# Optimization experiments

Hardware: AMD Instinct MI355X
Metric: run time of the kernel (lower is better)

## Reference

```python
import jax, jax.numpy as jnp
import numpy as np

N_NODES = 50000
N_EDGES = 800000
HIDDEN = 128
HEADS = 8
HEAD_DIM = HIDDEN // HEADS
N_REL = 64
SCALE = np.sqrt(HEAD_DIM).astype(np.float32)


def setup_inputs() -> dict:
    key = jax.random.key(0)
    ks = jax.random.split(key, 12)
    s = 1.0 / np.sqrt(2 * HIDDEN)
    s2 = 1.0 / np.sqrt(HIDDEN)
    return {
        "node_features": jax.random.normal(ks[0], (N_NODES, HIDDEN), jnp.float32),
        "query_embedding": jax.random.normal(ks[1], (1, HIDDEN), jnp.float32),
        "relation_embeddings": jax.random.normal(ks[2], (N_REL, HIDDEN), jnp.float32),
        "Wq": jax.random.uniform(ks[3], (2 * HIDDEN, HIDDEN), jnp.float32, -s, s),
        "bq": jnp.zeros((HIDDEN,), jnp.float32),
        "Wk": jax.random.uniform(ks[4], (2 * HIDDEN, HIDDEN), jnp.float32, -s, s),
        "bk": jnp.zeros((HIDDEN,), jnp.float32),
        "Wv": jax.random.uniform(ks[5], (HIDDEN, HIDDEN), jnp.float32, -s2, s2),
        "bv": jnp.zeros((HIDDEN,), jnp.float32),
        "Wo": jax.random.uniform(ks[6], (HIDDEN, HIDDEN), jnp.float32, -s2, s2),
        "bo": jnp.zeros((HIDDEN,), jnp.float32),
        "edge_index": jax.random.randint(ks[7], (2, N_EDGES), 0, N_NODES, jnp.int64),
        "edge_type": jax.random.randint(ks[8], (N_EDGES,), 0, N_REL, jnp.int64),
    }


def reference(node_features, query_embedding, relation_embeddings,
              Wq, bq, Wk, bk, Wv, bv, Wo, bo, edge_index, edge_type):
    n = node_features.shape[0]
    # expand query to all nodes and concat: [N, 2*hidden]
    q_exp = jnp.broadcast_to(query_embedding, (n, HIDDEN))
    nq = jnp.concatenate([node_features, q_exp], axis=-1)
    q = (nq @ Wq + bq).reshape(n, HEADS, HEAD_DIM)
    k = (nq @ Wk + bk).reshape(n, HEADS, HEAD_DIM)
    v = (node_features @ Wv + bv).reshape(n, HEADS, HEAD_DIM)

    src, dst = edge_index[0], edge_index[1]
    rel_bias = relation_embeddings[edge_type].reshape(-1, HEADS, HEAD_DIM)

    # edge-wise scores [E, heads]
    scores = jnp.sum(q[dst] * (k[src] + rel_bias), axis=-1) / SCALE

    # sparse softmax grouped by dst; torch init of max buffer is 0 -> clamp at 0
    seg_max = jax.ops.segment_max(scores, dst, num_segments=n)
    seg_max = jnp.maximum(seg_max, 0.0)
    exp_s = jnp.exp(scores - seg_max[dst])
    seg_sum = jax.ops.segment_sum(exp_s, dst, num_segments=n)
    attn = exp_s / (seg_sum[dst] + 1e-8)  # [E, heads]

    messages = attn[:, :, None] * v[src]  # [E, heads, head_dim]
    out = jax.ops.segment_sum(messages, dst, num_segments=n)  # [N, heads, head_dim]
    out = out.reshape(n, HIDDEN)
    return out @ Wo + bo
```

## Files before the change

### kernel.cpp

```cpp
#include <hip/hip_runtime.h>
#include <math.h>

#define N_NODES 50000
#define N_EDGES 800000
#define HID 128
#define HEADS 8
#define HDIM 16
#define CAP 96
#define CNT_BLOCKS 3125
#define QKV_BLOCKS 782
#define NFB_BLOCKS 3125

typedef __attribute__((ext_vector_type(8))) short short8;
typedef __attribute__((ext_vector_type(4))) float floatx4;

#if defined(__has_builtin)
#if __has_builtin(__builtin_amdgcn_fdot2_f32_bf16)
#define HAVE_DOT2 1
#endif
#endif
#ifndef HAVE_DOT2
#define HAVE_DOT2 0
#endif

#if HAVE_DOT2
typedef __attribute__((ext_vector_type(2))) __bf16 bf16x2;
__device__ __forceinline__ float dot2acc(unsigned int a, unsigned int b, float c) {
    return __builtin_amdgcn_fdot2_f32_bf16(__builtin_bit_cast(bf16x2, a),
                                           __builtin_bit_cast(bf16x2, b), c, false);
}
#endif

__device__ __forceinline__ float bf_lo(unsigned int d) { return __uint_as_float(d << 16); }
__device__ __forceinline__ float bf_hi(unsigned int d) { return __uint_as_float(d & 0xFFFF0000u); }
__device__ __forceinline__ unsigned short f2bf(float f) {
    unsigned int u = __float_as_uint(f);
    u = (u + 0x7FFFu + ((u >> 16) & 1u)) >> 16;
    return (unsigned short)u;
}
__device__ __forceinline__ unsigned int pack_bf2(float a, float b) {
    return (unsigned int)f2bf(a) | ((unsigned int)f2bf(b) << 16);
}

__global__ __launch_bounds__(256) void prep_kernel(
    const float* __restrict__ nf,
    const float* __restrict__ query, const float* __restrict__ rel,
    const float* __restrict__ Wq, const float* __restrict__ bq,
    const float* __restrict__ Wk, const float* __restrict__ bk,
    const float* __restrict__ Wv, const float* __restrict__ Wo,
    unsigned short* __restrict__ Wt, unsigned short* __restrict__ relbf,
    int* __restrict__ counts, float* __restrict__ bqe, float* __restrict__ bke,
    unsigned short* __restrict__ nfb) {
    __shared__ float fred[256];
    int b = blockIdx.x, tid = threadIdx.x;
    if (b >= 258) {
        int base = (b - 258) * 2048 + tid * 8;
        const float4* p = (const float4*)(nf + base);
        float4 a0 = p[0], a1 = p[1];
        short8 f;
        f[0] = (short)f2bf(a0.x); f[1] = (short)f2bf(a0.y);
        f[2] = (short)f2bf(a0.z); f[3] = (short)f2bf(a0.w);
        f[4] = (short)f2bf(a1.x); f[5] = (short)f2bf(a1.y);
        f[6] = (short)f2bf(a1.z); f[7] = (short)f2bf(a1.w);
        *(short8*)(nfb + base) = f;
        return;
    }
    if (b >= 256) {
        const float* W  = (b == 256) ? Wq : Wk;
        const float* bb = (b == 256) ? bq : bk;
        float* dst      = (b == 256) ? bqe : bke;
        int j = tid & 127;
        int half = tid >> 7;
        float a = 0.0f;
        int i0 = half * 64;
        for (int i = 0; i < 64; ++i) a += query[i0 + i] * W[(HID + i0 + i) * HID + j];
        fred[tid] = a;
        __syncthreads();
        if (half == 0) dst[j] = fred[j] + fred[128 + j] + bb[j];
        return;
    }
    int idx = b * 256 + tid;
    if (idx < N_NODES) counts[idx] = 0;
    if (idx < 64 * HID) relbf[idx] = f2bf(rel[idx]);
    int m = idx >> 14;
    int rem = idx & 16383;
    int n = rem >> 7, k = rem & 127;
    const float* W = (m == 0) ? Wq : (m == 1) ? Wk : (m == 2) ? Wv : Wo;
    Wt[idx] = f2bf(W[k * HID + n]);
}

__global__ __launch_bounds__(256) void bucket_kernel(
    const int* __restrict__ ei, const int* __restrict__ et,
    int* __restrict__ counts, unsigned int* __restrict__ slots) {
    int e = blockIdx.x * 256 + threadIdx.x;
    if (e < N_EDGES) {
        int dst = ei[N_EDGES + e];
        int pos = atomicAdd(&counts[dst], 1);
        if (pos < CAP)
            slots[(unsigned)dst * CAP + pos] =
                ((unsigned int)et[e] << 18) | (unsigned int)ei[e];
    }
}

__global__ __launch_bounds__(256) void qkv_kernel(
    const unsigned short* __restrict__ nfb, const unsigned short* __restrict__ Wt,
    const float* __restrict__ bqe, const float* __restrict__ bke, const float* __restrict__ bv,
    unsigned short* __restrict__ qb16, unsigned short* __restrict__ kv16) {
    int row0 = blockIdx.x * 64;
    int wave = threadIdx.x >> 6;
    int lane = threadIdx.x & 63;
    int col  = lane & 15;
    int quad = lane >> 4;

    short8 afr[4][4];
    #pragma unroll
    for (int t = 0; t < 4; ++t) {
        int arow = row0 + t * 16 + col;
        int asafe = (arow < N_NODES) ? arow : (N_NODES - 1);
        #pragma unroll
        for (int kk = 0; kk < 4; ++kk)
            afr[t][kk] = *(const short8*)(nfb + (size_t)asafe * HID + kk * 32 + quad * 8);
    }
    const float* biases[3] = {bqe, bke, bv};
    #pragma unroll
    for (int m = 0; m < 3; ++m) {
        const unsigned short* W = Wt + (size_t)m * HID * HID;
        #pragma unroll
        for (int nn = 0; nn < 2; ++nn) {
            int n = wave * 2 + nn;
            float b = biases[m][n * 16 + col];
            floatx4 acc[4];
            #pragma unroll
            for (int t = 0; t < 4; ++t) acc[t] = (floatx4){b, b, b, b};
            short8 bfr[4];
            #pragma unroll
            for (int kk = 0; kk < 4; ++kk)
                bfr[kk] = *(const short8*)(W + (size_t)(n * 16 + col) * HID + kk * 32 + quad * 8);
            #pragma unroll
            for (int kk = 0; kk < 4; ++kk)
                #pragma unroll
                for (int t = 0; t < 4; ++t)
                    acc[t] = __builtin_amdgcn_mfma_f32_16x16x32_bf16(afr[t][kk], bfr[kk], acc[t], 0, 0, 0);
            #pragma unroll
            for (int t = 0; t < 4; ++t) {
                #pragma unroll
                for (int i = 0; i < 4; ++i) {
                    int r = row0 + t * 16 + quad * 4 + i;
                    if (r < N_NODES) {
                        int c = n * 16 + col;
                        if (m == 0)      qb16[(size_t)r * HID + c] = f2bf(acc[t][i]);
                        else if (m == 1) kv16[(size_t)r * 256 + c] = f2bf(acc[t][i]);
                        else             kv16[(size_t)r * 256 + 128 + c] = f2bf(acc[t][i]);
                    }
                }
            }
        }
    }
}

__global__ __launch_bounds__(256) void attn_kernel(
    const unsigned int* __restrict__ qb, const unsigned int* __restrict__ kvu,
    const unsigned int* __restrict__ relu,
    const int* __restrict__ counts, const unsigned int* __restrict__ slots,
    unsigned int* __restrict__ abuf) {
    int node = blockIdx.x * 4 + (threadIdx.x >> 6);
    int lane = threadIdx.x & 63;
    int h = lane & 7;
    int hd = lane >> 3;
    int deg = counts[node];
    if (deg > CAP) deg = CAP;
    unsigned int rs = (unsigned)node * CAP;

    const uint4* qp = (const uint4*)(qb + (unsigned)node * 64 + h * 8);
    uint4 qa = qp[0], qc = qp[1];
#if !HAVE_DOT2
    float qf0 = bf_lo(qa.x), qf1 = bf_hi(qa.x), qf2 = bf_lo(qa.y), qf3 = bf_hi(qa.y);
    float qf4 = bf_lo(qa.z), qf5 = bf_hi(qa.z), qf6 = bf_lo(qa.w), qf7 = bf_hi(qa.w);
    float qf8 = bf_lo(qc.x), qf9 = bf_hi(qc.x), qf10 = bf_lo(qc.y), qf11 = bf_hi(qc.y);
    float qf12 = bf_lo(qc.z), qf13 = bf_hi(qc.z), qf14 = bf_lo(qc.w), qf15 = bf_hi(qc.w);
#endif

    int myel = hd;
    unsigned int pk = (myel < deg) ? slots[rs + myel] : 0u;
    float ssum = 0.0f, accx = 0.0f, accy = 0.0f;
    for (int base = 0; base < deg; base += 8) {
        int el = base + myel;
        int eln = el + 8;
        unsigned int pk_next = (eln < deg) ? slots[rs + eln] : 0u;
        unsigned int pw = 0u;
        if (el < deg) {
            unsigned int src = pk & 0x3FFFF;
            unsigned int etv = pk >> 18;
            const uint4* kp = (const uint4*)(kvu + (src << 7) + h * 8);
            uint4 ka = kp[0], kb = kp[1];
            const uint4* rp = (const uint4*)(relu + (etv << 6) + h * 8);
            uint4 ra = rp[0], rb = rp[1];
            float s;
#if HAVE_DOT2
            float s0 = dot2acc(qa.x, ka.x, 0.0f);
            float s1 = dot2acc(qa.y, ka.y, 0.0f);
            float s2 = dot2acc(qa.z, ka.z, 0.0f);
            float s3 = dot2acc(qa.w, ka.w, 0.0f);
            s0 = dot2acc(qc.x, kb.x, s0);
            s1 = dot2acc(qc.y, kb.y, s1);
            s2 = dot2acc(qc.z, kb.z, s2);
            s3 = dot2acc(qc.w, kb.w, s3);
            s0 = dot2acc(qa.x, ra.x, s0);
            s1 = dot2acc(qa.y, ra.y, s1);
            s2 = dot2acc(qa.z, ra.z, s2);
            s3 = dot2acc(qa.w, ra.w, s3);
            s0 = dot2acc(qc.x, rb.x, s0);
            s1 = dot2acc(qc.y, rb.y, s1);
            s2 = dot2acc(qc.z, rb.z, s2);
            s3 = dot2acc(qc.w, rb.w, s3);
            s = (s0 + s1) + (s2 + s3);
#else
            float s0 = qf0 * (bf_lo(ka.x) + bf_lo(ra.x)) + qf4 * (bf_lo(ka.z) + bf_lo(ra.z))
                     + qf8 * (bf_lo(kb.x) + bf_lo(rb.x)) + qf12 * (bf_lo(kb.z) + bf_lo(rb.z));
            float s1 = qf1 * (bf_hi(ka.x) + bf_hi(ra.x)) + qf5 * (bf_hi(ka.z) + bf_hi(ra.z))
                     + qf9 * (bf_hi(kb.x) + bf_hi(rb.x)) + qf13 * (bf_hi(kb.z) + bf_hi(rb.z));
            float s2 = qf2 * (bf_lo(ka.y) + bf_lo(ra.y)) + qf6 * (bf_lo(ka.w) + bf_lo(ra.w))
                     + qf10 * (bf_lo(kb.y) + bf_lo(rb.y)) + qf14 * (bf_lo(kb.w) + bf_lo(rb.w));
            float s3 = qf3 * (bf_hi(ka.y) + bf_hi(ra.y)) + qf7 * (bf_hi(ka.w) + bf_hi(ra.w))
                     + qf11 * (bf_hi(kb.y) + bf_hi(rb.y)) + qf15 * (bf_hi(kb.w) + bf_hi(rb.w));
            s = (s0 + s1) + (s2 + s3);
#endif
            float w = __expf(s * 0.25f);
            unsigned int wb = (unsigned int)f2bf(w);
            ssum += __uint_as_float(wb << 16);
            pw = (wb << 16) | src;
        }
        #pragma unroll
        for (int j = 0; j < 8; ++j) {
            unsigned int pj = __shfl(pw, j * 8 + hd);
            float wj = bf_hi(pj);
            unsigned int sj = pj & 0xFFFFu;
            unsigned int vp = kvu[(sj << 7) + 64 + lane];
            accx += wj * bf_lo(vp);
            accy += wj * bf_hi(vp);
        }
        pk = pk_next;
    }
    #pragma unroll
    for (int off = 8; off < 64; off <<= 1) ssum += __shfl_xor(ssum, off);
    float inv = 1.0f / (__shfl(ssum, hd) + 1e-8f);
    abuf[(unsigned)node * 64 + lane] = pack_bf2(accx * inv, accy * inv);
}

__global__ __launch_bounds__(256) void out_mfma_kernel(
    const unsigned short* __restrict__ abuf, const unsigned short* __restrict__ Wot,
    const float* __restrict__ bo, float* __restrict__ out) {
    int row0 = blockIdx.x * 64;
    int wave = threadIdx.x >> 6;
    int lane = threadIdx.x & 63;
    int col  = lane & 15;
    int quad = lane >> 4;

    short8 afr[4][4];
    #pragma unroll
    for (int t = 0; t < 4; ++t) {
        int arow = row0 + t * 16 + col;
        int asafe = (arow < N_NODES) ? arow : (N_NODES - 1);
        #pragma unroll
        for (int kk = 0; kk < 4; ++kk)
            afr[t][kk] = *(const short8*)(abuf + (size_t)asafe * HID + kk * 32 + quad * 8);
    }

    #pragma unroll
    for (int nn = 0; nn < 2; ++nn) {
        int n = wave * 2 + nn;
        float b = bo[n * 16 + col];
        floatx4 acc[4];
        #pragma unroll
        for (int t = 0; t < 4; ++t) acc[t] = (floatx4){b, b, b, b};
        short8 bfr[4];
        #pragma unroll
        for (int kk = 0; kk < 4; ++kk)
            bfr[kk] = *(const short8*)(Wot + (size_t)(n * 16 + col) * HID + kk * 32 + quad * 8);
        #pragma unroll
        for (int kk = 0; kk < 4; ++kk)
            #pragma unroll
            for (int t = 0; t < 4; ++t)
                acc[t] = __builtin_amdgcn_mfma_f32_16x16x32_bf16(afr[t][kk], bfr[kk], acc[t], 0, 0, 0);
        #pragma unroll
        for (int t = 0; t < 4; ++t) {
            #pragma unroll
            for (int i = 0; i < 4; ++i) {
                int r = row0 + t * 16 + quad * 4 + i;
                if (r < N_NODES) out[(size_t)r * HID + n * 16 + col] = acc[t][i];
            }
        }
    }
}

extern "C" void kernel_launch(void* const* d_in, const int* in_sizes, int n_in,
                              void* d_out, int out_size, void* d_ws, size_t ws_size,
                              hipStream_t stream) {
    const float* nf    = (const float*)d_in[0];
    const float* query = (const float*)d_in[1];
    const float* rel   = (const float*)d_in[2];
    const float* Wq    = (const float*)d_in[3];
    const float* bq    = (const float*)d_in[4];
    const float* Wk    = (const float*)d_in[5];
    const float* bk    = (const float*)d_in[6];
    const float* Wv    = (const float*)d_in[7];
    const float* bv    = (const float*)d_in[8];
    const float* Wo    = (const float*)d_in[9];
    const float* bo    = (const float*)d_in[10];
    const int*   ei    = (const int*)d_in[11];
    const int*   et    = (const int*)d_in[12];
    float* out = (float*)d_out;

    char* ws = (char*)d_ws;
    unsigned short* qb16 = (unsigned short*)ws; ws += (size_t)N_NODES * HID * 2;
    unsigned short* kv16 = (unsigned short*)ws; ws += (size_t)N_NODES * 256 * 2;
    unsigned int* abuf   = (unsigned int*)ws;   ws += (size_t)N_NODES * 64 * 4;
    float* bqe           = (float*)ws;          ws += 128 * 4;
    float* bke           = (float*)ws;          ws += 128 * 4;
    int* counts          = (int*)ws;            ws += (size_t)N_NODES * 4;
    unsigned int* slots  = (unsigned int*)ws;   ws += (size_t)N_NODES * CAP * 4;
    unsigned short* Wt   = (unsigned short*)ws; ws += (size_t)4 * HID * HID * 2;
    unsigned short* relbf = (unsigned short*)ws; ws += (size_t)64 * HID * 2;
    unsigned short* nfb  = (unsigned short*)ws; ws += (size_t)N_NODES * HID * 2;

    prep_kernel<<<258 + NFB_BLOCKS, 256, 0, stream>>>(nf, query, rel, Wq, bq, Wk, bk, Wv, Wo,
                                                      Wt, relbf, counts, bqe, bke, nfb);
    bucket_kernel<<<CNT_BLOCKS, 256, 0, stream>>>(ei, et, counts, slots);
    qkv_kernel<<<QKV_BLOCKS, 256, 0, stream>>>(nfb, Wt, bqe, bke, bv, qb16, kv16);
    attn_kernel<<<N_NODES / 4, 256, 0, stream>>>(
        (const unsigned int*)qb16, (const unsigned int*)kv16,
        (const unsigned int*)relbf, counts, slots, abuf);
    out_mfma_kernel<<<QKV_BLOCKS, 256, 0, stream>>>(
        (const unsigned short*)abuf, Wt + (size_t)3 * HID * HID, bo, out);
}
```

Measured before the change: 251.0 us.

## Fuse edge bucketing into prep kernel and vectorize attention V gather

Merges the edge bucketing pass into the prep kernel, with each thread handling four edges through int4 loads, and clears the counts buffer with a memset instead of inside prep. In the attention kernel, each lane now gathers 16 bytes of V per edge instead of 4, and partial sums are reduced across lane quarters with shuffles, with a single uint4 store per row. The goal is to cut one kernel launch, use wider memory transactions and shorten the per-edge gather loop. The cost is extra shuffle reductions and more accumulator registers, and bucket atomics now run concurrently with the conversion blocks.

Measured after the change: 246.5 us. No clear change (-1.8%).

```diff
diff --git a/kernel.cpp b/kernel.cpp
--- a/kernel.cpp
+++ b/kernel.cpp
@@ -7,9 +7,9 @@
 #define HEADS 8
 #define HDIM 16
 #define CAP 96
-#define CNT_BLOCKS 3125
 #define QKV_BLOCKS 782
 #define NFB_BLOCKS 3125
+#define BUCKET_BLOCKS 782
 
 typedef __attribute__((ext_vector_type(8))) short short8;
 typedef __attribute__((ext_vector_type(4))) float floatx4;
@@ -42,19 +42,40 @@
     return (unsigned int)f2bf(a) | ((unsigned int)f2bf(b) << 16);
 }
 
-__global__ __launch_bounds__(256) void prep_kernel(
+__global__ __launch_bounds__(256) void prep_bucket_kernel(
     const float* __restrict__ nf,
     const float* __restrict__ query, const float* __restrict__ rel,
     const float* __restrict__ Wq, const float* __restrict__ bq,
     const float* __restrict__ Wk, const float* __restrict__ bk,
     const float* __restrict__ Wv, const float* __restrict__ Wo,
+    const int* __restrict__ ei, const int* __restrict__ et,
+    int* __restrict__ counts, unsigned int* __restrict__ slots,
     unsigned short* __restrict__ Wt, unsigned short* __restrict__ relbf,
-    int* __restrict__ counts, float* __restrict__ bqe, float* __restrict__ bke,
+    float* __restrict__ bqe, float* __restrict__ bke,
     unsigned short* __restrict__ nfb) {
     __shared__ float fred[256];
     int b = blockIdx.x, tid = threadIdx.x;
-    if (b >= 258) {
-        int base = (b - 258) * 2048 + tid * 8;
+    if (b < BUCKET_BLOCKS) {
+        int t4 = b * 256 + tid;
+        if (t4 < N_EDGES / 4) {
+            int e0 = t4 * 4;
+            int4 dd = *(const int4*)(ei + N_EDGES + e0);
+            int4 ss = *(const int4*)(ei + e0);
+            int4 tt = *(const int4*)(et + e0);
+            int p0 = atomicAdd(&counts[dd.x], 1);
+            int p1 = atomicAdd(&counts[dd.y], 1);
+            int p2 = atomicAdd(&counts[dd.z], 1);
+            int p3 = atomicAdd(&counts[dd.w], 1);
+            if (p0 < CAP) slots[(unsigned)dd.x * CAP + p0] = ((unsigned)tt.x << 18) | (unsigned)ss.x;
+            if (p1 < CAP) slots[(unsigned)dd.y * CAP + p1] = ((unsigned)tt.y << 18) | (unsigned)ss.y;
+            if (p2 < CAP) slots[(unsigned)dd.z * CAP + p2] = ((unsigned)tt.z << 18) | (unsigned)ss.z;
+            if (p3 < CAP) slots[(unsigned)dd.w * CAP + p3] = ((unsigned)tt.w << 18) | (unsigned)ss.w;
+        }
+        return;
+    }
+    b -= BUCKET_BLOCKS;
+    if (b < NFB_BLOCKS) {
+        int base = b * 2048 + tid * 8;
         const float4* p = (const float4*)(nf + base);
         float4 a0 = p[0], a1 = p[1];
         short8 f;
@@ -65,7 +86,18 @@
         *(short8*)(nfb + base) = f;
         return;
     }
-    if (b >= 256) {
+    b -= NFB_BLOCKS;
+    if (b < 256) {
+        int idx = b * 256 + tid;
+        if (idx < 64 * HID) relbf[idx] = f2bf(rel[idx]);
+        int m = idx >> 14;
+        int rem = idx & 16383;
+        int n = rem >> 7, k = rem & 127;
+        const float* W = (m == 0) ? Wq : (m == 1) ? Wk : (m == 2) ? Wv : Wo;
+        Wt[idx] = f2bf(W[k * HID + n]);
+        return;
+    }
+    {
         const float* W  = (b == 256) ? Wq : Wk;
         const float* bb = (b == 256) ? bq : bk;
         float* dst      = (b == 256) ? bqe : bke;
@@ -77,28 +109,6 @@
         fred[tid] = a;
         __syncthreads();
         if (half == 0) dst[j] = fred[j] + fred[128 + j] + bb[j];
-        return;
-    }
-    int idx = b * 256 + tid;
-    if (idx < N_NODES) counts[idx] = 0;
-    if (idx < 64 * HID) relbf[idx] = f2bf(rel[idx]);
-    int m = idx >> 14;
-    int rem = idx & 16383;
-    int n = rem >> 7, k = rem & 127;
-    const float* W = (m == 0) ? Wq : (m == 1) ? Wk : (m == 2) ? Wv : Wo;
-    Wt[idx] = f2bf(W[k * HID + n]);
-}
-
-__global__ __launch_bounds__(256) void bucket_kernel(
-    const int* __restrict__ ei, const int* __restrict__ et,
-    int* __restrict__ counts, unsigned int* __restrict__ slots) {
-    int e = blockIdx.x * 256 + threadIdx.x;
-    if (e < N_EDGES) {
-        int dst = ei[N_EDGES + e];
-        int pos = atomicAdd(&counts[dst], 1);
-        if (pos < CAP)
-            slots[(unsigned)dst * CAP + pos] =
-                ((unsigned int)et[e] << 18) | (unsigned int)ei[e];
     }
 }
 
@@ -167,6 +177,8 @@
     int lane = threadIdx.x & 63;
     int h = lane & 7;
     int hd = lane >> 3;
+    int qi = lane & 15;
+    int quarter = lane >> 4;
     int deg = counts[node];
     if (deg > CAP) deg = CAP;
     unsigned int rs = (unsigned)node * CAP;
@@ -182,7 +194,8 @@
 
     int myel = hd;
     unsigned int pk = (myel < deg) ? slots[rs + myel] : 0u;
-    float ssum = 0.0f, accx = 0.0f, accy = 0.0f;
+    float ssum = 0.0f;
+    float acc[8] = {0.f, 0.f, 0.f, 0.f, 0.f, 0.f, 0.f, 0.f};
     for (int base = 0; base < deg; base += 8) {
         int el = base + myel;
         int eln = el + 8;
@@ -231,20 +244,35 @@
             pw = (wb << 16) | src;
         }
         #pragma unroll
-        for (int j = 0; j < 8; ++j) {
-            unsigned int pj = __shfl(pw, j * 8 + hd);
+        for (int t = 0; t < 2; ++t) {
+            int j = t * 4 + quarter;
+            unsigned int pj = __shfl(pw, j * 8 + (qi >> 1));
             float wj = bf_hi(pj);
             unsigned int sj = pj & 0xFFFFu;
-            unsigned int vp = kvu[(sj << 7) + 64 + lane];
-            accx += wj * bf_lo(vp);
-            accy += wj * bf_hi(vp);
+            uint4 v = *(const uint4*)(kvu + (sj << 7) + 64 + qi * 4);
+            acc[0] += wj * bf_lo(v.x); acc[1] += wj * bf_hi(v.x);
+            acc[2] += wj * bf_lo(v.y); acc[3] += wj * bf_hi(v.y);
+            acc[4] += wj * bf_lo(v.z); acc[5] += wj * bf_hi(v.z);
+            acc[6] += wj * bf_lo(v.w); acc[7] += wj * bf_hi(v.w);
         }
         pk = pk_next;
     }
     #pragma unroll
     for (int off = 8; off < 64; off <<= 1) ssum += __shfl_xor(ssum, off);
-    float inv = 1.0f / (__shfl(ssum, hd) + 1e-8f);
-    abuf[(unsigned)node * 64 + lane] = pack_bf2(accx * inv, accy * inv);
+    #pragma unroll
+    for (int k = 0; k < 8; ++k) {
+        acc[k] += __shfl_xor(acc[k], 16);
+        acc[k] += __shfl_xor(acc[k], 32);
+    }
+    float inv = 1.0f / (__shfl(ssum, qi >> 1) + 1e-8f);
+    if (lane < 16) {
+        uint4 o;
+        o.x = pack_bf2(acc[0] * inv, acc[1] * inv);
+        o.y = pack_bf2(acc[2] * inv, acc[3] * inv);
+        o.z = pack_bf2(acc[4] * inv, acc[5] * inv);
+        o.w = pack_bf2(acc[6] * inv, acc[7] * inv);
+        *(uint4*)(abuf + (unsigned)node * 64 + qi * 4) = o;
+    }
 }
 
 __global__ __launch_bounds__(256) void out_mfma_kernel(
@@ -323,9 +351,10 @@
     unsigned short* relbf = (unsigned short*)ws; ws += (size_t)64 * HID * 2;
     unsigned short* nfb  = (unsigned short*)ws; ws += (size_t)N_NODES * HID * 2;
 
-    prep_kernel<<<258 + NFB_BLOCKS, 256, 0, stream>>>(nf, query, rel, Wq, bq, Wk, bk, Wv, Wo,
-                                                      Wt, relbf, counts, bqe, bke, nfb);
-    bucket_kernel<<<CNT_BLOCKS, 256, 0, stream>>>(ei, et, counts, slots);
+    hipMemsetAsync(counts, 0, (size_t)N_NODES * 4, stream);
+    prep_bucket_kernel<<<BUCKET_BLOCKS + NFB_BLOCKS + 258, 256, 0, stream>>>(
+        nf, query, rel, Wq, bq, Wk, bk, Wv, Wo, ei, et,
+        counts, slots, Wt, relbf, bqe, bke, nfb);
     qkv_kernel<<<QKV_BLOCKS, 256, 0, stream>>>(nfb, Wt, bqe, bke, bv, qb16, kv16);
     attn_kernel<<<N_NODES / 4, 256, 0, stream>>>(
         (const unsigned int*)qb16, (const unsigned int*)kv16,
```
